# Kernel tuning notes

Hardware: AMD Instinct MI355X
Metric: run time of the kernel (lower is better)

The kernel has to match this reference:

```python
import jax, jax.numpy as jnp
import numpy as np

N_EMBD = 512
HEAD_SIZE = 64
END_TOKEN = 32000  # == vocab_size


def setup_inputs() -> dict:
    key = jax.random.key(0)
    k1, k2, k3, k4, k5 = jax.random.split(key, 5)
    B, T = 16, 2048
    x = jax.random.normal(k1, (B, T, N_EMBD), dtype=jnp.float32)
    idx = jax.random.randint(k2, (B, T), 0, END_TOKEN)  # never hits END_TOKEN
    s = 1.0 / np.sqrt(N_EMBD)
    Wk = jax.random.normal(k3, (N_EMBD, HEAD_SIZE), dtype=jnp.float32) * s
    Wq = jax.random.normal(k4, (N_EMBD, HEAD_SIZE), dtype=jnp.float32) * s
    Wv = jax.random.normal(k5, (N_EMBD, HEAD_SIZE), dtype=jnp.float32) * s
    return {"x": x, "Wk": Wk, "Wq": Wq, "Wv": Wv, "idx": idx}


def reference(x, Wk, Wq, Wv, idx):
    B, T, C = x.shape
    k = x @ Wk  # [B,T,H]
    q = x @ Wq
    v = x @ Wv
    # end-token mask: zero out query rows at positions >= first end-token position
    is_end = idx == END_TOKEN                       # [B,T]
    has_end = jnp.any(is_end, axis=1)               # [B]
    first_end = jnp.argmax(is_end, axis=1)          # [B], 0 if none
    pos = jnp.arange(T)
    row_ok = jnp.where(has_end[:, None], pos[None, :] < first_end[:, None], True)  # [B,T]
    causal = jnp.tril(jnp.ones((T, T), dtype=bool))
    mask = causal[None, :, :] & row_ok[:, :, None]  # [B,T,T]
    # NOTE: original scales by C**-0.5 with C = n_embd, not head_size
    wei = jnp.einsum('bqh,bkh->bqk', q, k) * (C ** -0.5)
    wei = jnp.where(mask, wei, -jnp.inf)
    wei = jax.nn.softmax(wei, axis=-1)
    out = jnp.einsum('bqk,bkh->bqh', wei, v)  # [B,T,H]
    return out
```

## Files before the change

### kernel.cpp

```cpp
#include <hip/hip_runtime.h>
#include <hip/hip_bf16.h>


#define B_ 16
#define T_ 2048
#define C_ 512
#define LOG2E 1.4426950408889634f

typedef __attribute__((ext_vector_type(4))) float f32x4;
typedef __attribute__((ext_vector_type(8))) short bf16x8;
typedef __attribute__((ext_vector_type(4))) unsigned int u32x4;

__device__ inline unsigned short f2bf(float f) {
    unsigned int u = __builtin_bit_cast(unsigned int, f);
    u += 0x7fff + ((u >> 16) & 1);
    return (unsigned short)(u >> 16);
}

__device__ inline unsigned int cvt_pk_bf16(float lo, float hi) {
    unsigned int r;
    asm("v_cvt_pk_bf16_f32 %0, %1, %2" : "=v"(r) : "v"(lo), "v"(hi));
    return r;
}

__device__ inline f32x4 mfma16(bf16x8 a, bf16x8 b, f32x4 c) {
    return __builtin_amdgcn_mfma_f32_16x16x32_bf16(a, b, c, 0, 0, 0);
}

__global__ void prep_kernel(const float* __restrict__ Wk, const float* __restrict__ Wq,
                            const float* __restrict__ Wv, unsigned short* __restrict__ Wt,
                            int* __restrict__ fe) {
    if (blockIdx.x == 384) {
        if (threadIdx.x < B_) fe[threadIdx.x] = T_;
        return;
    }
    int id = blockIdx.x * 256 + threadIdx.x;
    int n = id >> 9, k = id & 511;
    int mtx = n >> 6, nl = n & 63;
    const float* W = (mtx == 0) ? Wk : ((mtx == 1) ? Wq : Wv);
    float v = W[k * 64 + nl];
    if (mtx == 1) v *= 0.04419417382415922f;
    Wt[n * 512 + k] = f2bf(v);
}

__global__ void scan_kernel(const int* __restrict__ idx, int* __restrict__ fe) {
    int i = blockIdx.x * 256 + threadIdx.x;
    if (idx[i] == 32000) atomicMin(&fe[i >> 11], i & 2047);
}

__global__ __launch_bounds__(256) void qkv_kernel(
        const float* __restrict__ x, const unsigned short* __restrict__ Wt,
        unsigned short* __restrict__ Qm, unsigned short* __restrict__ Km,
        unsigned short* __restrict__ Vt) {
    __shared__ __align__(16) char smem[32768];
    unsigned short* xs  = (unsigned short*)smem;
    unsigned short* wsh = (unsigned short*)(smem + 8192);
    unsigned short* co  = (unsigned short*)smem;
    unsigned short* vco = (unsigned short*)(smem + 17408);

    int tid = threadIdx.x, wave = tid >> 6, lane = tid & 63;
    int m16 = lane & 15, quad = lane >> 4;
    int row0 = blockIdx.x * 64;

    int xrow[2], xcol[2], wrow[6], wcol[6];
#pragma unroll
    for (int i = 0; i < 2; i++) { int u = tid + i * 256; xrow[i] = u >> 3; xcol[i] = (u & 7) * 8; }
#pragma unroll
    for (int i = 0; i < 6; i++) { int u = tid + i * 256; wrow[i] = u >> 3; wcol[i] = (u & 7) * 8; }

    f32x4 xa[2][2]; bf16x8 wr[6];
#pragma unroll
    for (int i = 0; i < 2; i++) {
        const f32x4* p = (const f32x4*)(x + (long)(row0 + xrow[i]) * C_ + xcol[i]);
        xa[i][0] = p[0]; xa[i][1] = p[1];
    }
#pragma unroll
    for (int i = 0; i < 6; i++) wr[i] = *(const bf16x8*)&Wt[wrow[i] * C_ + wcol[i]];

    f32x4 ka[4], qa[4], va[4];
#pragma unroll
    for (int i = 0; i < 4; i++) {
        ka[i] = (f32x4){0.f, 0.f, 0.f, 0.f};
        qa[i] = (f32x4){0.f, 0.f, 0.f, 0.f};
        va[i] = (f32x4){0.f, 0.f, 0.f, 0.f};
    }

    for (int kb = 0; kb < C_; kb += 64) {
        __syncthreads();
#pragma unroll
        for (int i = 0; i < 2; i++) {
            u32x4 t;
            t[0] = cvt_pk_bf16(xa[i][0][0], xa[i][0][1]);
            t[1] = cvt_pk_bf16(xa[i][0][2], xa[i][0][3]);
            t[2] = cvt_pk_bf16(xa[i][1][0], xa[i][1][1]);
            t[3] = cvt_pk_bf16(xa[i][1][2], xa[i][1][3]);
            *(u32x4*)&xs[xrow[i] * 64 + (xcol[i] ^ ((xrow[i] & 7) * 8))] = t;
        }
#pragma unroll
        for (int i = 0; i < 6; i++)
            *(bf16x8*)&wsh[wrow[i] * 64 + (wcol[i] ^ ((wrow[i] & 7) * 8))] = wr[i];
        __syncthreads();
        int kn = kb + 64;
        if (kn < C_) {
#pragma unroll
            for (int i = 0; i < 2; i++) {
                const f32x4* p = (const f32x4*)(x + (long)(row0 + xrow[i]) * C_ + kn + xcol[i]);
                xa[i][0] = p[0]; xa[i][1] = p[1];
            }
#pragma unroll
            for (int i = 0; i < 6; i++) wr[i] = *(const bf16x8*)&Wt[wrow[i] * C_ + kn + wcol[i]];
        }
#pragma unroll
        for (int ks = 0; ks < 2; ks++) {
            int ko = ks * 32 + quad * 8;
            bf16x8 xf[4];
#pragma unroll
            for (int mt = 0; mt < 4; mt++) {
                int ar = mt * 16 + m16;
                xf[mt] = *(const bf16x8*)&xs[ar * 64 + (ko ^ ((ar & 7) * 8))];
            }
            int kr = wave * 16 + m16, qr = 64 + wave * 16 + m16, vr = 128 + wave * 16 + m16;
            bf16x8 wk = *(const bf16x8*)&wsh[kr * 64 + (ko ^ ((kr & 7) * 8))];
            bf16x8 wq = *(const bf16x8*)&wsh[qr * 64 + (ko ^ ((qr & 7) * 8))];
            bf16x8 wv = *(const bf16x8*)&wsh[vr * 64 + (ko ^ ((vr & 7) * 8))];
#pragma unroll
            for (int mt = 0; mt < 4; mt++) ka[mt] = mfma16(xf[mt], wk, ka[mt]);
#pragma unroll
            for (int mt = 0; mt < 4; mt++) qa[mt] = mfma16(xf[mt], wq, qa[mt]);
#pragma unroll
            for (int mt = 0; mt < 4; mt++) va[mt] = mfma16(wv, xf[mt], va[mt]);
        }
    }
    __syncthreads();

#pragma unroll
    for (int mt = 0; mt < 4; mt++) {
        int trow = mt * 16 + quad * 4;
#pragma unroll
        for (int r = 0; r < 4; r++) {
            co[(trow + r) * 136 + wave * 16 + m16]      = f2bf(ka[mt][r]);
            co[(trow + r) * 136 + 64 + wave * 16 + m16] = f2bf(qa[mt][r]);
            vco[wave * 1152 + (quad * 4 + r) * 72 + mt * 16 + m16] = f2bf(va[mt][r]);
        }
    }
    __syncthreads();
#pragma unroll
    for (int i = 0; i < 4; i++) {
        int u = tid + i * 256; int tok = u >> 4; int fg = u & 15;
        bf16x8 vv = *(const bf16x8*)&co[tok * 136 + fg * 8];
        unsigned short* dst = (fg < 8) ? Km : Qm;
        *(bf16x8*)&dst[(long)(row0 + tok) * 64 + (fg & 7) * 8] = vv;
    }
    int bb = row0 >> 11, tl = row0 & 2047;
#pragma unroll
    for (int i = 0; i < 2; i++) {
        int u = lane + i * 64; int hl = u >> 3; int tg = u & 7;
        bf16x8 vv = *(const bf16x8*)&vco[wave * 1152 + hl * 72 + tg * 8];
        *(bf16x8*)&Vt[((long)bb * 64 + wave * 16 + hl) * T_ + tl + tg * 8] = vv;
    }
}

__global__ __launch_bounds__(512, 4) void attn_kernel(
        const unsigned short* __restrict__ Qm, const unsigned short* __restrict__ Km,
        const unsigned short* __restrict__ Vt, const int* __restrict__ fe,
        float* __restrict__ out) {
    __shared__ __align__(16) unsigned short Klds[2][2][64 * 64];
    __shared__ __align__(16) unsigned short Vlds[2][2][64 * 64];
    __shared__ __align__(16) unsigned short Plds[8][16 * 64];

    int id = blockIdx.x;
    int j = id & 255, hi = id >> 8;
    int qt = hi ? 31 - (j >> 3) : (j >> 3);
    int b = (j & 7) | (hi << 3);

    int tid = threadIdx.x, wave = tid >> 6, lane = tid & 63;
    int g = wave >> 2, wg = wave & 3;
    int m16 = lane & 15, quad = lane >> 4;
    int row0 = qt * 64;
    long bT = (long)b * T_;

    int n = qt + 1;
    int n0 = (n + 1) >> 1;
    int n1 = n - n0;
    int ng = g ? n1 : n0;
    int kbase = g ? n0 : 0;
    int nloop = n0;

    int gtid = wg * 64 + lane;
    int srow[2], sk8[2], ssw[2];
#pragma unroll
    for (int c = 0; c < 2; c++) {
        int cc = gtid + c * 256;
        srow[c] = cc >> 3; sk8[c] = (cc & 7) * 8;
        ssw[c] = sk8[c] ^ ((srow[c] & 7) * 8);
    }

    const unsigned short* qp = Qm + (bT + row0 + wg * 16 + m16) * 64;
    bf16x8 qf0 = *(const bf16x8*)(qp + quad * 8);
    bf16x8 qf1 = *(const bf16x8*)(qp + 32 + quad * 8);

    f32x4 o[5];
#pragma unroll
    for (int h = 0; h < 5; h++) o[h] = (f32x4){0.f, 0.f, 0.f, 0.f};
    float mi[4];
#pragma unroll
    for (int r = 0; r < 4; r++) mi[r] = -INFINITY;
    int qloc = row0 + wg * 16 + quad * 4;

    bf16x8 onesb;
    {
        short ov = (m16 == 0) ? (short)0x3F80 : (short)0;
#pragma unroll
        for (int jj = 0; jj < 8; jj++) onesb[jj] = ov;
    }

    unsigned short (*Kg)[64 * 64] = Klds[g];
    unsigned short (*Vg)[64 * 64] = Vlds[g];

    bf16x8 kp[2], vp[2];
    if (ng > 0) {
        long c0 = (long)kbase * 64;
#pragma unroll
        for (int c = 0; c < 2; c++) {
            kp[c] = *(const bf16x8*)&Km[(bT + c0 + srow[c]) * 64 + sk8[c]];
            vp[c] = *(const bf16x8*)&Vt[((long)b * 64 + srow[c]) * T_ + c0 + sk8[c]];
        }
#pragma unroll
        for (int c = 0; c < 2; c++) {
            *(bf16x8*)&Kg[0][srow[c] * 64 + ssw[c]] = kp[c];
            *(bf16x8*)&Vg[0][srow[c] * 64 + ssw[c]] = vp[c];
        }
    }

    for (int it = 0; it < nloop; ++it) {
        int cur = it & 1;
        bool active = it < ng;
        int kt = kbase + it;
        bool pf = active && (it + 1 < ng);
        if (pf) {
            long cn = (long)(kt + 1) * 64;
#pragma unroll
            for (int c = 0; c < 2; c++) {
                kp[c] = *(const bf16x8*)&Km[(bT + cn + srow[c]) * 64 + sk8[c]];
                vp[c] = *(const bf16x8*)&Vt[((long)b * 64 + srow[c]) * T_ + cn + sk8[c]];
            }
        }
        __syncthreads();
        if (active) {
            const unsigned short* Kb = Kg[cur];
            const unsigned short* Vb = Vg[cur];

            f32x4 s[4];
#pragma unroll
            for (int ns = 0; ns < 4; ns++) {
                int krow = ns * 16 + m16;
                int swz = (krow & 7) * 8;
                bf16x8 kf0 = *(const bf16x8*)&Kb[krow * 64 + ((quad * 8) ^ swz)];
                bf16x8 kf1 = *(const bf16x8*)&Kb[krow * 64 + ((32 + quad * 8) ^ swz)];
                f32x4 z = (f32x4){0.f, 0.f, 0.f, 0.f};
                z = mfma16(qf0, kf0, z);
                z = mfma16(qf1, kf1, z);
                s[ns] = z;
            }

            bool diag = (kt == qt);
#pragma unroll
            for (int r = 0; r < 4; r++) {
                int qpos = qloc + r;
                if (diag) {
#pragma unroll
                    for (int ns = 0; ns < 4; ns++) {
                        int nn = kt * 64 + ns * 16 + m16;
                        if (nn > qpos) s[ns][r] = -INFINITY;
                    }
                }
                float mx = fmaxf(fmaxf(s[0][r], s[1][r]), fmaxf(s[2][r], s[3][r]));
                mx = fmaxf(mx, mi[r]);
#pragma unroll
                for (int off = 1; off < 16; off <<= 1)
                    mx = fmaxf(mx, __shfl_xor(mx, off));
                float alpha = exp2f((mi[r] - mx) * LOG2E);
                mi[r] = mx;
#pragma unroll
                for (int ns = 0; ns < 4; ns++)
                    s[ns][r] = exp2f((s[ns][r] - mx) * LOG2E);
#pragma unroll
                for (int h = 0; h < 5; h++) o[h][r] *= alpha;
            }

            unsigned short* pw = Plds[wave];
#pragma unroll
            for (int ns = 0; ns < 4; ns++)
#pragma unroll
                for (int r = 0; r < 4; r++) {
                    int mrow = quad * 4 + r;
                    int nn = ns * 16 + m16;
                    pw[mrow * 64 + (nn ^ ((mrow & 7) * 8))] = f2bf(s[ns][r]);
                }

            int aswz = (m16 & 7) * 8;
            bf16x8 pa0 = *(const bf16x8*)&pw[m16 * 64 + ((quad * 8) ^ aswz)];
            bf16x8 pa1 = *(const bf16x8*)&pw[m16 * 64 + ((32 + quad * 8) ^ aswz)];
#pragma unroll
            for (int hs = 0; hs < 4; hs++) {
                int vrow = hs * 16 + m16;
                int vswz = (vrow & 7) * 8;
                bf16x8 vb0 = *(const bf16x8*)&Vb[vrow * 64 + ((quad * 8) ^ vswz)];
                bf16x8 vb1 = *(const bf16x8*)&Vb[vrow * 64 + ((32 + quad * 8) ^ vswz)];
                o[hs] = mfma16(pa0, vb0, o[hs]);
                o[hs] = mfma16(pa1, vb1, o[hs]);
            }
            o[4] = mfma16(pa0, onesb, o[4]);
            o[4] = mfma16(pa1, onesb, o[4]);
        }
        if (pf) {
            int nxt = 1 - cur;
#pragma unroll
            for (int c = 0; c < 2; c++) {
                *(bf16x8*)&Kg[nxt][srow[c] * 64 + ssw[c]] = kp[c];
                *(bf16x8*)&Vg[nxt][srow[c] * 64 + ssw[c]] = vp[c];
            }
        }
    }

    __syncthreads();
    float* Po = (float*)&Klds[0][0][0];
    float* Pm = Po + 64 * 68;
    float* Pl = Pm + 64;
    if (g == 1) {
#pragma unroll
        for (int r = 0; r < 4; r++) {
            int row = wg * 16 + quad * 4 + r;
#pragma unroll
            for (int hs = 0; hs < 4; hs++)
                Po[row * 68 + hs * 16 + m16] = o[hs][r];
            if (m16 == 0) { Pm[row] = mi[r]; Pl[row] = o[4][r]; }
        }
    }
    __syncthreads();
    if (g == 0) {
        int feb = fe[b];
#pragma unroll
        for (int r = 0; r < 4; r++) {
            int row = wg * 16 + quad * 4 + r;
            int t = row0 + row;
            float m1v = Pm[row], l1v = Pl[row];
            float mm = fmaxf(mi[r], m1v);
            float a0 = exp2f((mi[r] - mm) * LOG2E);
            float a1 = exp2f((m1v - mm) * LOG2E);
            float l0 = __shfl(o[4][r], lane & 48);
            float inv = 1.0f / (l0 * a0 + l1v * a1);
            bool dead = (t >= feb);
#pragma unroll
            for (int hs = 0; hs < 4; hs++) {
                float val = dead ? __builtin_nanf("")
                                 : (o[hs][r] * a0 + Po[row * 68 + hs * 16 + m16] * a1) * inv;
                out[(bT + t) * 64 + hs * 16 + m16] = val;
            }
        }
    }
}

extern "C" void kernel_launch(void* const* d_in, const int* in_sizes, int n_in,
                              void* d_out, int out_size, void* d_ws, size_t ws_size,
                              hipStream_t stream) {
    const float* x  = (const float*)d_in[0];
    const float* Wk = (const float*)d_in[1];
    const float* Wq = (const float*)d_in[2];
    const float* Wv = (const float*)d_in[3];
    const int* idx  = (const int*)d_in[4];
    float* out = (float*)d_out;

    char* ws = (char*)d_ws;
    int* fe            = (int*)ws;
    unsigned short* Wt = (unsigned short*)(ws + 1024);
    unsigned short* Qm = (unsigned short*)(ws + 262144);
    unsigned short* Km = (unsigned short*)(ws + 262144 + 4194304);
    unsigned short* Vt = (unsigned short*)(ws + 262144 + 8388608);

    prep_kernel<<<385, 256, 0, stream>>>(Wk, Wq, Wv, Wt, fe);
    scan_kernel<<<128, 256, 0, stream>>>(idx, fe);
    qkv_kernel<<<512, 256, 0, stream>>>(x, Wt, Qm, Km, Vt);
    attn_kernel<<<512, 512, 0, stream>>>(Qm, Km, Vt, fe, out);
}
```

Before: 153.4 us.

## Merge end-token scan into prep kernel and fold log2e into Q scale

```diff
diff --git a/kernel.cpp b/kernel.cpp
--- a/kernel.cpp
+++ b/kernel.cpp
@@ -5,7 +5,6 @@
 #define B_ 16
 #define T_ 2048
 #define C_ 512
-#define LOG2E 1.4426950408889634f
 
 typedef __attribute__((ext_vector_type(4))) float f32x4;
 typedef __attribute__((ext_vector_type(8))) short bf16x8;
@@ -29,9 +28,20 @@
 
 __global__ void prep_kernel(const float* __restrict__ Wk, const float* __restrict__ Wq,
                             const float* __restrict__ Wv, unsigned short* __restrict__ Wt,
-                            int* __restrict__ fe) {
-    if (blockIdx.x == 384) {
-        if (threadIdx.x < B_) fe[threadIdx.x] = T_;
+                            const int* __restrict__ idx, int* __restrict__ pbmin) {
+    if (blockIdx.x >= 384) {
+        __shared__ int wmin[4];
+        int bid = blockIdx.x - 384;
+        int i = bid * 256 + threadIdx.x;
+        int val = (idx[i] == 32000) ? (i & 2047) : T_;
+#pragma unroll
+        for (int off = 1; off < 64; off <<= 1)
+            val = min(val, __shfl_xor(val, off));
+        int wave = threadIdx.x >> 6, lane = threadIdx.x & 63;
+        if (lane == 0) wmin[wave] = val;
+        __syncthreads();
+        if (threadIdx.x == 0)
+            pbmin[bid] = min(min(wmin[0], wmin[1]), min(wmin[2], wmin[3]));
         return;
     }
     int id = blockIdx.x * 256 + threadIdx.x;
@@ -39,13 +49,8 @@
     int mtx = n >> 6, nl = n & 63;
     const float* W = (mtx == 0) ? Wk : ((mtx == 1) ? Wq : Wv);
     float v = W[k * 64 + nl];
-    if (mtx == 1) v *= 0.04419417382415922f;
+    if (mtx == 1) v *= 0.0637587166f;
     Wt[n * 512 + k] = f2bf(v);
-}
-
-__global__ void scan_kernel(const int* __restrict__ idx, int* __restrict__ fe) {
-    int i = blockIdx.x * 256 + threadIdx.x;
-    if (idx[i] == 32000) atomicMin(&fe[i >> 11], i & 2047);
 }
 
 __global__ __launch_bounds__(256) void qkv_kernel(
@@ -162,7 +167,7 @@
 
 __global__ __launch_bounds__(512, 4) void attn_kernel(
         const unsigned short* __restrict__ Qm, const unsigned short* __restrict__ Km,
-        const unsigned short* __restrict__ Vt, const int* __restrict__ fe,
+        const unsigned short* __restrict__ Vt, const int* __restrict__ pbmin,
         float* __restrict__ out) {
     __shared__ __align__(16) unsigned short Klds[2][2][64 * 64];
     __shared__ __align__(16) unsigned short Vlds[2][2][64 * 64];
@@ -237,6 +242,7 @@
         bool active = it < ng;
         int kt = kbase + it;
         bool pf = active && (it + 1 < ng);
+        __syncthreads();
         if (pf) {
             long cn = (long)(kt + 1) * 64;
 #pragma unroll
@@ -245,7 +251,6 @@
                 vp[c] = *(const bf16x8*)&Vt[((long)b * 64 + srow[c]) * T_ + cn + sk8[c]];
             }
         }
-        __syncthreads();
         if (active) {
             const unsigned short* Kb = Kg[cur];
             const unsigned short* Vb = Vg[cur];
@@ -279,11 +284,11 @@
 #pragma unroll
                 for (int off = 1; off < 16; off <<= 1)
                     mx = fmaxf(mx, __shfl_xor(mx, off));
-                float alpha = exp2f((mi[r] - mx) * LOG2E);
+                float alpha = exp2f(mi[r] - mx);
                 mi[r] = mx;
 #pragma unroll
                 for (int ns = 0; ns < 4; ns++)
-                    s[ns][r] = exp2f((s[ns][r] - mx) * LOG2E);
+                    s[ns][r] = exp2f(s[ns][r] - mx);
 #pragma unroll
                 for (int h = 0; h < 5; h++) o[h][r] *= alpha;
             }
@@ -339,15 +344,17 @@
     }
     __syncthreads();
     if (g == 0) {
-        int feb = fe[b];
+        int feb = T_;
+#pragma unroll
+        for (int c = 0; c < 8; c++) feb = min(feb, pbmin[b * 8 + c]);
 #pragma unroll
         for (int r = 0; r < 4; r++) {
             int row = wg * 16 + quad * 4 + r;
             int t = row0 + row;
             float m1v = Pm[row], l1v = Pl[row];
             float mm = fmaxf(mi[r], m1v);
-            float a0 = exp2f((mi[r] - mm) * LOG2E);
-            float a1 = exp2f((m1v - mm) * LOG2E);
+            float a0 = exp2f(mi[r] - mm);
+            float a1 = exp2f(m1v - mm);
             float l0 = __shfl(o[4][r], lane & 48);
             float inv = 1.0f / (l0 * a0 + l1v * a1);
             bool dead = (t >= feb);
@@ -372,14 +379,13 @@
     float* out = (float*)d_out;
 
     char* ws = (char*)d_ws;
-    int* fe            = (int*)ws;
+    int* pbmin         = (int*)ws;
     unsigned short* Wt = (unsigned short*)(ws + 1024);
     unsigned short* Qm = (unsigned short*)(ws + 262144);
     unsigned short* Km = (unsigned short*)(ws + 262144 + 4194304);
     unsigned short* Vt = (unsigned short*)(ws + 262144 + 8388608);
 
-    prep_kernel<<<385, 256, 0, stream>>>(Wk, Wq, Wv, Wt, fe);
-    scan_kernel<<<128, 256, 0, stream>>>(idx, fe);
+    prep_kernel<<<512, 256, 0, stream>>>(Wk, Wq, Wv, Wt, idx, pbmin);
     qkv_kernel<<<512, 256, 0, stream>>>(x, Wt, Qm, Km, Vt);
-    attn_kernel<<<512, 512, 0, stream>>>(Qm, Km, Vt, fe, out);
-}
+    attn_kernel<<<512, 512, 0, stream>>>(Qm, Km, Vt, pbmin, out);
+}
```

New measurement: 152.6 us. No clear change (-0.5%).
